# Kernel optimization log

Hardware: AMD Instinct MI355X
Metric: run time of the kernel (lower is better)

## Reference

```python
import jax, jax.numpy as jnp
import numpy as np


def _gcn_conv(x, W, b, src, dst, num_nodes):
    """PyG GCNConv with default args: add self-loops + symmetric normalization.
    x: [N, F_in], W: [F_in, F_out], b: [F_out], src/dst: [E] (self-loops already included).
    """
    h = x @ W  # [N, F_out]
    # in-degree of destination nodes (counting self-loops)
    ones = jnp.ones_like(dst, dtype=h.dtype)
    deg = jax.ops.segment_sum(ones, dst, num_segments=num_nodes)  # [N]
    dinv = jnp.where(deg > 0, jax.lax.rsqrt(jnp.maximum(deg, 1.0)), 0.0)
    norm = dinv[src] * dinv[dst]  # [E]
    msgs = h[src] * norm[:, None]  # [E, F_out] gather + scale
    out = jax.ops.segment_sum(msgs, dst, num_segments=num_nodes)  # scatter-add
    return out + b


def setup_inputs() -> dict:
    key = jax.random.key(0)
    k1, k2, k3, k4 = jax.random.split(key, 4)
    N, E, F_IN, HID = 100000, 1600000, 128, 64
    x = jax.random.normal(k1, (N, F_IN), dtype=jnp.float32)
    edge_index = jax.random.randint(k2, (2, E), 0, N, dtype=jnp.int64)
    W1 = jax.random.normal(k3, (F_IN, HID), dtype=jnp.float32) * (1.0 / np.sqrt(F_IN))
    b1 = jnp.zeros((HID,), dtype=jnp.float32)
    W2 = jax.random.normal(k4, (HID, 1), dtype=jnp.float32) * (1.0 / np.sqrt(HID))
    b2 = jnp.zeros((1,), dtype=jnp.float32)
    return {"x": x, "edge_index": edge_index, "W1": W1, "b1": b1, "W2": W2, "b2": b2}


def reference(x, edge_index, W1, b1, W2, b2):
    N = x.shape[0]
    # add self-loops (GCNConv default add_self_loops=True)
    loop = jnp.arange(N, dtype=edge_index.dtype)
    src = jnp.concatenate([edge_index[0], loop])
    dst = jnp.concatenate([edge_index[1], loop])
    h = jax.nn.relu(_gcn_conv(x, W1, b1, src, dst, N))
    out = _gcn_conv(h, W2, b2, src, dst, N)
    return out  # [N, 1]
```

## Files before the change

kernel.cpp:

```cpp
#include <hip/hip_runtime.h>
#include <hip/hip_fp16.h>

#define F_IN 128
#define HID  64
#define CAP  96
#define CSHIFT 9
#define CNODES 512
#define NC_MAX 256
#define CCHUNK 4096
#define BCAPC 8960

__launch_bounds__(256)
__global__ void k_coarse(const int* __restrict__ src, const int* __restrict__ dst,
                         int* __restrict__ acur, int* __restrict__ ent, int E, int nc) {
    __shared__ int s_cnt[NC_MAX];
    __shared__ int s_gb[NC_MAX];
    __shared__ int s_bump[NC_MAX];
    int t = threadIdx.x;
    int e0 = blockIdx.x * CCHUNK;
    int n = E - e0; if (n > CCHUNK) n = CCHUNK;

    for (int i = t; i < nc; i += 256) { s_cnt[i] = 0; s_bump[i] = 0; }
    __syncthreads();
    for (int i = t; i < n; i += 256)
        atomicAdd(&s_cnt[dst[e0 + i] >> CSHIFT], 1);
    __syncthreads();
    if (t < nc) {
        int c = s_cnt[t];
        s_gb[t] = (c > 0) ? atomicAdd(&acur[t], c) : 0;
    }
    __syncthreads();
    for (int i = t; i < n; i += 256) {
        int d = dst[e0 + i], s = src[e0 + i];
        int b = d >> CSHIFT;
        int p = s_gb[b] + atomicAdd(&s_bump[b], 1);
        if (p < BCAPC) ent[(size_t)b * BCAPC + p] = (s << CSHIFT) | (d & (CNODES - 1));
    }
}

__launch_bounds__(1024)
__global__ void k_fillc(const int* __restrict__ acur, const int* __restrict__ ent,
                        int* __restrict__ counts, int* __restrict__ csrc, int N) {
    __shared__ int lcnt[CNODES];
    int b = blockIdx.x, t = threadIdx.x;
    if (t < CNODES) lcnt[t] = 0;
    __syncthreads();
    int base = b * CNODES;
    int cnt = acur[b]; if (cnt > BCAPC) cnt = BCAPC;
    const int* ep = ent + (size_t)b * BCAPC;
    for (int i = t; i < cnt; i += 1024) {
        int v = ep[i];
        int ld = v & (CNODES - 1), s = v >> CSHIFT;
        int p = atomicAdd(&lcnt[ld], 1);
        if (p < CAP) csrc[(size_t)(base + ld) * CAP + p] = s;
    }
    __syncthreads();
    if (t < CNODES && base + t < N) {
        int cc = lcnt[t]; if (cc > CAP) cc = CAP;
        counts[base + t] = cc;
    }
}

__launch_bounds__(256, 8)
__global__ void k_gemm(const float* __restrict__ x, const float* __restrict__ W1,
                       const int* __restrict__ counts, __half* __restrict__ hn, int N) {
    int t = threadIdx.x;
    int lane = t & 63;
    int c0 = __builtin_amdgcn_readfirstlane(t >> 6) * 16;
    int r0 = blockIdx.x * 64;
    int row = r0 + lane;
    int rr = (row < N) ? row : (N - 1);

    const float* xr = x + (size_t)rr * F_IN;

    float acc[16];
#pragma unroll
    for (int c = 0; c < 16; ++c) acc[c] = 0.f;

    for (int k = 0; k < F_IN; k += 4) {
        float4 xv = *(const float4*)&xr[k];
        const float* wr = W1 + (size_t)k * HID + c0;
#pragma unroll
        for (int c = 0; c < 16; ++c) {
            float a = acc[c];
            a = fmaf(xv.x, wr[c], a);
            a = fmaf(xv.y, wr[HID + c], a);
            a = fmaf(xv.z, wr[2 * HID + c], a);
            a = fmaf(xv.w, wr[3 * HID + c], a);
            acc[c] = a;
        }
    }

    if (row < N) {
        float di = rsqrtf((float)(counts[row] + 1));
        __half* hp = hn + (size_t)row * HID + c0;
        unsigned int us[8];
#pragma unroll
        for (int c = 0; c < 16; c += 2) {
            __half2 h2 = __floats2half2_rn(acc[c] * di, acc[c + 1] * di);
            us[c >> 1] = *(unsigned int*)&h2;
        }
        *(uint4*)&hp[0] = make_uint4(us[0], us[1], us[2], us[3]);
        *(uint4*)&hp[8] = make_uint4(us[4], us[5], us[6], us[7]);
    }
}

__device__ inline void accum8(float acc[8], int4 raw, float w) {
    int v[4] = { raw.x, raw.y, raw.z, raw.w };
#pragma unroll
    for (int h = 0; h < 4; ++h) {
        __half2 h2 = *(__half2*)&v[h];
        float2 f = __half22float2(h2);
        acc[2 * h]     = fmaf(w, f.x, acc[2 * h]);
        acc[2 * h + 1] = fmaf(w, f.y, acc[2 * h + 1]);
    }
}

__launch_bounds__(256)
__global__ void k_gather1(const int* __restrict__ csrc, const int* __restrict__ counts,
                          const __half* __restrict__ hn, const float* __restrict__ b1,
                          const float* __restrict__ W2, float* __restrict__ zn, int N) {
    int lane = threadIdx.x & 63;
    int g    = (lane >> 3) & 3;
    int li   = lane & 7;
    int r = blockIdx.x * 8 + ((threadIdx.x >> 6) << 1) + (lane >> 5);
    int rr = (r < N) ? r : (N - 1);
    int cnt = (r < N) ? counts[rr] : 0;

    const int4* cs4 = (const int4*)(csrc + (size_t)rr * CAP);
    size_t lo = (size_t)li * 8;

    float acc[8];
#pragma unroll
    for (int c = 0; c < 8; ++c) acc[c] = 0.f;

    {
        int4 sA = cs4[g];
        int idx[4]; float w[4];
        idx[0] = sA.x; idx[1] = sA.y; idx[2] = sA.z; idx[3] = sA.w;
#pragma unroll
        for (int k = 0; k < 4; ++k) {
            int e = 4 * g + k;
            bool v = (e < cnt);
            idx[k] = v ? idx[k] : rr;
            w[k]   = v ? 1.f : 0.f;
        }
        int4 raw[4];
#pragma unroll
        for (int k = 0; k < 4; ++k)
            raw[k] = *(const int4*)&hn[(size_t)idx[k] * HID + lo];
#pragma unroll
        for (int k = 0; k < 4; ++k) accum8(acc, raw[k], w[k]);
    }

    int cntO = __shfl_xor(cnt, 32, 64);
    int cmax = (cnt > cntO) ? cnt : cntO;

    if (cmax > 16) {
        int4 sB = cs4[4 + g];
        int idx[4]; float w[4];
        idx[0] = sB.x; idx[1] = sB.y; idx[2] = sB.z; idx[3] = sB.w;
#pragma unroll
        for (int k = 0; k < 4; ++k) {
            int e = 16 + 4 * g + k;
            bool v = (e < cnt);
            idx[k] = v ? idx[k] : rr;
            w[k]   = v ? 1.f : 0.f;
        }
        int4 raw[4];
#pragma unroll
        for (int k = 0; k < 4; ++k)
            raw[k] = *(const int4*)&hn[(size_t)idx[k] * HID + lo];
#pragma unroll
        for (int k = 0; k < 4; ++k) accum8(acc, raw[k], w[k]);
    }

    for (int c = 32; c < cmax; c += 16) {
        int4 s = cs4[(c >> 2) + g];
        int idx[4]; float w[4];
        idx[0] = s.x; idx[1] = s.y; idx[2] = s.z; idx[3] = s.w;
#pragma unroll
        for (int k = 0; k < 4; ++k) {
            int e = c + 4 * g + k;
            bool v = (e < cnt);
            idx[k] = v ? idx[k] : rr;
            w[k]   = v ? 1.f : 0.f;
        }
        int4 raw[4];
#pragma unroll
        for (int k = 0; k < 4; ++k)
            raw[k] = *(const int4*)&hn[(size_t)idx[k] * HID + lo];
#pragma unroll
        for (int k = 0; k < 4; ++k) accum8(acc, raw[k], w[k]);
    }

#pragma unroll
    for (int c = 0; c < 8; ++c) {
        acc[c] += __shfl_xor(acc[c], 8, 64);
        acc[c] += __shfl_xor(acc[c], 16, 64);
    }

    int4 rawR = *(const int4*)&hn[(size_t)rr * HID + lo];
    accum8(acc, rawR, 1.f);

    float di = rsqrtf((float)(cnt + 1));
    float4 b0 = *(const float4*)&b1[li * 8];
    float4 b4 = *(const float4*)&b1[li * 8 + 4];
    float4 w0 = *(const float4*)&W2[li * 8];
    float4 w4 = *(const float4*)&W2[li * 8 + 4];

    float p = fmaxf(fmaf(di, acc[0], b0.x), 0.f) * w0.x
            + fmaxf(fmaf(di, acc[1], b0.y), 0.f) * w0.y
            + fmaxf(fmaf(di, acc[2], b0.z), 0.f) * w0.z
            + fmaxf(fmaf(di, acc[3], b0.w), 0.f) * w0.w
            + fmaxf(fmaf(di, acc[4], b4.x), 0.f) * w4.x
            + fmaxf(fmaf(di, acc[5], b4.y), 0.f) * w4.y
            + fmaxf(fmaf(di, acc[6], b4.z), 0.f) * w4.z
            + fmaxf(fmaf(di, acc[7], b4.w), 0.f) * w4.w;

    p += __shfl_xor(p, 1, 64);
    p += __shfl_xor(p, 2, 64);
    p += __shfl_xor(p, 4, 64);

    if ((lane & 31) == 0 && r < N) zn[r] = p * di;
}

__global__ void k_gather2(const int* __restrict__ csrc, const int* __restrict__ counts,
                          const float* __restrict__ zn, const float* __restrict__ b2,
                          float* __restrict__ out, int N) {
    int t = blockIdx.x * blockDim.x + threadIdx.x;
    int r = t >> 4, li = t & 15;
    if (r >= N) return;
    size_t beg = (size_t)r * CAP;
    int cnt = counts[r];
    float acc = 0.f;
    for (int j = li; j < cnt; j += 16) {
        acc += zn[csrc[beg + j]];
    }
    acc += __shfl_xor(acc, 1, 64);
    acc += __shfl_xor(acc, 2, 64);
    acc += __shfl_xor(acc, 4, 64);
    acc += __shfl_xor(acc, 8, 64);
    if (li == 0) {
        float di = rsqrtf((float)(cnt + 1));
        out[r] = di * (acc + zn[r]) + b2[0];
    }
}

extern "C" void kernel_launch(void* const* d_in, const int* in_sizes, int n_in,
                              void* d_out, int out_size, void* d_ws, size_t ws_size,
                              hipStream_t stream) {
    const float* x  = (const float*)d_in[0];
    const int*   ei = (const int*)d_in[1];
    const float* W1 = (const float*)d_in[2];
    const float* b1 = (const float*)d_in[3];
    const float* W2 = (const float*)d_in[4];
    const float* b2 = (const float*)d_in[5];
    float* out = (float*)d_out;

    const int N = in_sizes[0] / F_IN;
    const int E = in_sizes[1] / 2;
    const int* src = ei;
    const int* dst = ei + E;

    const int nc = (N + CNODES - 1) / CNODES;
    const int NBKT = (N + 63) / 64;

    char* ws = (char*)d_ws;
    size_t off = 0;
    auto alloc = [&](size_t bytes) { void* p = ws + off; off += (bytes + 255) & ~255ULL; return p; };
    int*    acur   = (int*)   alloc((size_t)nc * 4);
    int*    counts = (int*)   alloc((size_t)N * 4);
    float*  zn     = (float*) alloc((size_t)N * 4);
    int*    ent    = (int*)   alloc((size_t)nc * BCAPC * 4);
    __half* hn     = (__half*)alloc((size_t)N * HID * 2);
    int*    csrc   = (int*)   alloc((size_t)N * CAP * 4);

    hipMemsetAsync(acur, 0, (size_t)nc * 4, stream);

    const int coarseBlks = (E + CCHUNK - 1) / CCHUNK;
    k_coarse<<<coarseBlks, 256, 0, stream>>>(src, dst, acur, ent, E, nc);
    k_fillc<<<nc, 1024, 0, stream>>>(acur, ent, counts, csrc, N);
    k_gemm<<<NBKT, 256, 0, stream>>>(x, W1, counts, hn, N);
    k_gather1<<<(N + 7) / 8, 256, 0, stream>>>(csrc, counts, hn, b1, W2, zn, N);
    k_gather2<<<((size_t)N * 16 + 255) / 256, 256, 0, stream>>>(csrc, counts, zn, b2, out, N);
}
```

Baseline: 197.3 us.

## Compute first-layer GEMM with split-bf16 MFMA instead of scalar FP32 FMAs

Replaces the scalar FP32 FMA loop of the x@W1 GEMM with MFMA 16x16x32 bf16 instructions. Both x and W1 are split into high and low bf16 parts, and four MFMAs per tile keep accuracy close to FP32. A small pre-kernel builds the transposed bf16 hi/lo copies of W1 on every call. The aim is to move the GEMM's compute to the matrix cores. In exchange the output writes become scattered 2-byte half stores instead of 16-byte vector stores, and the kernel adds one extra launch.

```diff
diff --git a/kernel.cpp b/kernel.cpp
--- a/kernel.cpp
+++ b/kernel.cpp
@@ -9,6 +9,17 @@
 #define NC_MAX 256
 #define CCHUNK 4096
 #define BCAPC 8960
+
+typedef short s16x8 __attribute__((ext_vector_type(8)));
+typedef float f32x4 __attribute__((ext_vector_type(4)));
+
+__device__ inline unsigned short bf16rne(float f) {
+    unsigned u = __float_as_uint(f);
+    return (unsigned short)((u + 0x7FFFu + ((u >> 16) & 1u)) >> 16);
+}
+__device__ inline float bf16tof(unsigned short h) {
+    return __uint_as_float(((unsigned)h) << 16);
+}
 
 __launch_bounds__(256)
 __global__ void k_coarse(const int* __restrict__ src, const int* __restrict__ dst,
@@ -61,47 +72,76 @@
     }
 }
 
-__launch_bounds__(256, 8)
-__global__ void k_gemm(const float* __restrict__ x, const float* __restrict__ W1,
+__launch_bounds__(256)
+__global__ void k_wsplit(const float* __restrict__ W1, unsigned short* __restrict__ W1hT,
+                         unsigned short* __restrict__ W1lT) {
+    int id = blockIdx.x * 256 + threadIdx.x;
+    int k = id >> 6, c = id & 63;
+    float f = W1[id];
+    unsigned short h = bf16rne(f);
+    unsigned short l = bf16rne(f - bf16tof(h));
+    W1hT[c * F_IN + k] = h;
+    W1lT[c * F_IN + k] = l;
+}
+
+__launch_bounds__(256)
+__global__ void k_gemm(const float* __restrict__ x,
+                       const unsigned short* __restrict__ W1hT,
+                       const unsigned short* __restrict__ W1lT,
                        const int* __restrict__ counts, __half* __restrict__ hn, int N) {
     int t = threadIdx.x;
     int lane = t & 63;
-    int c0 = __builtin_amdgcn_readfirstlane(t >> 6) * 16;
-    int r0 = blockIdx.x * 64;
-    int row = r0 + lane;
-    int rr = (row < N) ? row : (N - 1);
-
-    const float* xr = x + (size_t)rr * F_IN;
-
-    float acc[16];
-#pragma unroll
-    for (int c = 0; c < 16; ++c) acc[c] = 0.f;
-
-    for (int k = 0; k < F_IN; k += 4) {
-        float4 xv = *(const float4*)&xr[k];
-        const float* wr = W1 + (size_t)k * HID + c0;
-#pragma unroll
-        for (int c = 0; c < 16; ++c) {
-            float a = acc[c];
-            a = fmaf(xv.x, wr[c], a);
-            a = fmaf(xv.y, wr[HID + c], a);
-            a = fmaf(xv.z, wr[2 * HID + c], a);
-            a = fmaf(xv.w, wr[3 * HID + c], a);
-            acc[c] = a;
-        }
-    }
-
-    if (row < N) {
-        float di = rsqrtf((float)(counts[row] + 1));
-        __half* hp = hn + (size_t)row * HID + c0;
-        unsigned int us[8];
-#pragma unroll
-        for (int c = 0; c < 16; c += 2) {
-            __half2 h2 = __floats2half2_rn(acc[c] * di, acc[c + 1] * di);
-            us[c >> 1] = *(unsigned int*)&h2;
-        }
-        *(uint4*)&hp[0] = make_uint4(us[0], us[1], us[2], us[3]);
-        *(uint4*)&hp[8] = make_uint4(us[4], us[5], us[6], us[7]);
+    int wid = t >> 6;
+    int r0w = blockIdx.x * 64 + wid * 16;
+    int arow = r0w + (lane & 15);
+    int ar = (arow < N) ? arow : (N - 1);
+    int kq = lane >> 4;
+
+    const float* xr = x + (size_t)ar * F_IN + kq * 8;
+    int coff = (lane & 15) * F_IN + kq * 8;
+
+    f32x4 acc[4];
+#pragma unroll
+    for (int nt = 0; nt < 4; ++nt) acc[nt] = (f32x4){0.f, 0.f, 0.f, 0.f};
+
+#pragma unroll
+    for (int kt = 0; kt < 4; ++kt) {
+        float4 xa = *(const float4*)(xr + kt * 32);
+        float4 xb = *(const float4*)(xr + kt * 32 + 4);
+        float xf[8] = {xa.x, xa.y, xa.z, xa.w, xb.x, xb.y, xb.z, xb.w};
+        s16x8 ah, al;
+#pragma unroll
+        for (int j = 0; j < 8; ++j) {
+            unsigned short h = bf16rne(xf[j]);
+            ah[j] = (short)h;
+            al[j] = (short)bf16rne(xf[j] - bf16tof(h));
+        }
+        int kb = coff + kt * 32;
+#pragma unroll
+        for (int nt = 0; nt < 4; ++nt) {
+            s16x8 bh = *(const s16x8*)(W1hT + nt * 16 * F_IN + kb);
+            s16x8 bl = *(const s16x8*)(W1lT + nt * 16 * F_IN + kb);
+            acc[nt] = __builtin_amdgcn_mfma_f32_16x16x32_bf16(ah, bh, acc[nt], 0, 0, 0);
+            acc[nt] = __builtin_amdgcn_mfma_f32_16x16x32_bf16(al, bh, acc[nt], 0, 0, 0);
+            acc[nt] = __builtin_amdgcn_mfma_f32_16x16x32_bf16(ah, bl, acc[nt], 0, 0, 0);
+            acc[nt] = __builtin_amdgcn_mfma_f32_16x16x32_bf16(al, bl, acc[nt], 0, 0, 0);
+        }
+    }
+
+    int rbase = r0w + (lane >> 4) * 4;
+    if (rbase >= N) return;
+    int4 c4 = *(const int4*)(counts + rbase);
+    int cj[4] = {c4.x, c4.y, c4.z, c4.w};
+#pragma unroll
+    for (int j = 0; j < 4; ++j) {
+        int row = rbase + j;
+        if (row < N) {
+            float di = rsqrtf((float)(cj[j] + 1));
+            __half* hp = hn + (size_t)row * HID + (lane & 15);
+#pragma unroll
+            for (int nt = 0; nt < 4; ++nt)
+                hp[nt * 16] = __float2half_rn(acc[nt][j] * di);
+        }
     }
 }
 
@@ -272,6 +312,8 @@
     int*    acur   = (int*)   alloc((size_t)nc * 4);
     int*    counts = (int*)   alloc((size_t)N * 4);
     float*  zn     = (float*) alloc((size_t)N * 4);
+    unsigned short* W1hT = (unsigned short*) alloc((size_t)HID * F_IN * 2);
+    unsigned short* W1lT = (unsigned short*) alloc((size_t)HID * F_IN * 2);
     int*    ent    = (int*)   alloc((size_t)nc * BCAPC * 4);
     __half* hn     = (__half*)alloc((size_t)N * HID * 2);
     int*    csrc   = (int*)   alloc((size_t)N * CAP * 4);
@@ -279,9 +321,10 @@
     hipMemsetAsync(acur, 0, (size_t)nc * 4, stream);
 
     const int coarseBlks = (E + CCHUNK - 1) / CCHUNK;
+    k_wsplit<<<32, 256, 0, stream>>>(W1, W1hT, W1lT);
     k_coarse<<<coarseBlks, 256, 0, stream>>>(src, dst, acur, ent, E, nc);
     k_fillc<<<nc, 1024, 0, stream>>>(acur, ent, counts, csrc, N);
-    k_gemm<<<NBKT, 256, 0, stream>>>(x, W1, counts, hn, N);
+    k_gemm<<<NBKT, 256, 0, stream>>>(x, W1hT, W1lT, counts, hn, N);
     k_gather1<<<(N + 7) / 8, 256, 0, stream>>>(csrc, counts, hn, b1, W2, zn, N);
     k_gather2<<<((size_t)N * 16 + 255) / 256, 256, 0, stream>>>(csrc, counts, zn, b2, out, N);
 }
```

Result: slower. 202.5 us (+2.6%).
